# Kernel optimization log

Hardware: AMD Instinct MI355X
Metric: run time of the kernel (lower is better)

The kernel has to match this reference:

```python
import jax, jax.numpy as jnp
import numpy as np

DT = 0.01  # integrator base timestep (init kwarg)
DT_SCALE = 1.0


def setup_inputs() -> dict:
    key = jax.random.key(0)
    kx, kv, kf, ku, kw = jax.random.split(key, 5)
    B, D, R = 8192, 1024, 256
    scale = 1.0 / np.sqrt(D)
    return {
        "x": jax.random.normal(kx, (B, D), jnp.float32),
        "v": jax.random.normal(kv, (B, D), jnp.float32),
        "force": jax.random.normal(kf, (B, D), jnp.float32) * 0.1,
        "U": jax.random.normal(ku, (R, D), jnp.float32) * scale,
        "W": jax.random.normal(kw, (R, D), jnp.float32) * scale,
        "steps": 4,
    }


def _christoffel(v, x, U, W):
    # Low-rank Christoffel contraction Gamma(v, v; x):
    #   h = tanh(x W^T)   [B, r]  (position-dependent gating)
    #   q = v W^T         [B, r]  (velocity projection)
    #   Gamma = (h * q^2) U  [B, d]
    h = jnp.tanh(x @ W.T)
    q = v @ W.T
    return (h * q * q) @ U


def reference(x, v, force, U, W, steps):
    # topology_id == 0 (Euclidean): apply_boundary is the identity.
    dt = DT * DT_SCALE

    def dynamics(cx, cv):
        return -_christoffel(cv, cx, U, W) + force

    cx, cv = x, v
    for _ in range(steps):  # steps is a static Python int
        dx1 = cv
        dv1 = dynamics(cx, cv)
        v2 = cv + 0.5 * dt * dv1
        x2 = cx + 0.5 * dt * dx1
        dx2 = v2
        dv2 = dynamics(x2, v2)
        v3 = cv + 0.5 * dt * dv2
        x3 = cx + 0.5 * dt * dx2
        dx3 = v3
        dv3 = dynamics(x3, v3)
        v4 = cv + dt * dv3
        x4 = cx + dt * dx3
        dx4 = v4
        dv4 = dynamics(x4, v4)
        cx = cx + (dt / 6.0) * (dx1 + 2 * dx2 + 2 * dx3 + dx4)
        cv = cv + (dt / 6.0) * (dv1 + 2 * dv2 + 2 * dv3 + dv4)
    return (cx, cv)
```

## Files before the change

### kernel.cpp

```cpp
#include <hip/hip_runtime.h>
#include <hip/hip_bf16.h>
#include <hip/hip_fp8.h>


typedef __attribute__((ext_vector_type(8))) short bf16x8;
typedef __attribute__((ext_vector_type(4))) short bf16x4;
typedef __attribute__((ext_vector_type(4))) float f32x4;
typedef unsigned short us;
typedef unsigned char uc;

#define MFMA16 __builtin_amdgcn_mfma_f32_16x16x32_bf16
#define MFMA8  __builtin_amdgcn_mfma_f32_16x16x32_fp8_fp8

namespace {
constexpr int kB = 8192;
constexpr int kD = 1024;
constexpr int kR = 256;
constexpr int kBM = 16;
constexpr float kDt = 0.01f;
}

__device__ __forceinline__ us f2bf(float f) {
  __hip_bfloat16 h = __float2bfloat16(f);
  union { __hip_bfloat16 b; us u; } c; c.b = h;
  return c.u;
}
__device__ __forceinline__ unsigned pack2(float a, float b) {
  union { __hip_bfloat162 h; unsigned u; } c;
  c.h = __float22bfloat162_rn(float2{a, b});
  return c.u;
}
__device__ __forceinline__ float plo(unsigned u) {
  union { unsigned u; float f; } w; w.u = (u & 0xFFFFu) << 16; return w.f;
}
__device__ __forceinline__ float phi(unsigned u) {
  union { unsigned u; float f; } w; w.u = u & 0xFFFF0000u; return w.f;
}
__device__ __forceinline__ uc f2e4(float f) {
  __hip_fp8_e4m3 h(f);
  union { __hip_fp8_storage_t s; uc u; } c; c.s = h.__x;
  return c.u;
}
__device__ __forceinline__ bf16x4 pack4(float4 a) {
  union { bf16x4 v; __hip_bfloat162 h[2]; } u;
  u.h[0] = __float22bfloat162_rn(float2{a.x, a.y});
  u.h[1] = __float22bfloat162_rn(float2{a.z, a.w});
  return u.v;
}
__device__ __forceinline__ float ftanh(float x) {
  float e = __expf(2.f * x);
  return 1.f - 2.f / (e + 1.f);
}

__global__ void prep_wu(const float* __restrict__ U, const float* __restrict__ W,
                        us* __restrict__ Wb, us* __restrict__ Ub,
                        us* __restrict__ Wf, us* __restrict__ Uf) {
  int i = blockIdx.x * blockDim.x + threadIdx.x;
  if (i < kR * kD) {
    const int r = i >> 10, k = i & 1023;
    const us wb = f2bf(W[i]), ub = f2bf(U[i]);
    Wb[i] = wb; Ub[i] = ub;
    Wf[(((size_t)(r >> 4) * 32 + (k >> 5)) << 9) +
       (((((k >> 3) & 3) << 4) | (r & 15)) << 3) + (k & 7)] = wb;
    Uf[(((size_t)(k >> 4) * 8 + (r >> 5)) << 9) +
       (((((r >> 3) & 3) << 4) | (k & 15)) << 3) + (r & 7)] = ub;
  }
}

__global__ __launch_bounds__(256) void prep_g(const us* __restrict__ Wb,
                                              const us* __restrict__ Ub,
                                              uc* __restrict__ Gf8) {
  const int tid = threadIdx.x;
  const int w = tid >> 6, l = tid & 63;
  const int l15 = l & 15, l4 = l >> 4;
  const int n1 = (blockIdx.x >> 3) * 32 + (w >> 1) * 16;
  const int k1 = (blockIdx.x & 7) * 32 + (w & 1) * 16;
  f32x4 acc = {0.f, 0.f, 0.f, 0.f};
  const us* wp = Wb + (size_t)(n1 + l15) * kD + l4 * 8;
  const us* up = Ub + (size_t)(k1 + l15) * kD + l4 * 8;
#pragma unroll 8
  for (int kk = 0; kk < 32; ++kk) {
    bf16x8 aw = *(const bf16x8*)(wp + kk * 32);
    bf16x8 bu = *(const bf16x8*)(up + kk * 32);
    acc = MFMA16(aw, bu, acc, 0, 0, 0);
  }
#pragma unroll
  for (int j = 0; j < 4; ++j) {
    const int n = n1 + l4 * 4 + j, k = k1 + l15;
    Gf8[((size_t)((n >> 4) * 8 + (k >> 5)) << 9) +
        ((((k >> 3) & 3) * 16 + (n & 15)) << 3) + (k & 7)] = f2e4(64.f * acc[j]);
  }
}

__global__ __launch_bounds__(1024, 4) void fused_kernel(
    const us* __restrict__ Wf, const uc* __restrict__ Gf8, const us* __restrict__ Uf,
    const float* __restrict__ xin, const float* __restrict__ vin,
    const float* __restrict__ force,
    float* __restrict__ cxo, float* __restrict__ cvo) {
  __shared__ __align__(16) us stg[24576];
  __shared__ __align__(16) uc ct8[2][4096];

  const int tid = threadIdx.x;
  const int w = tid >> 6;
  const int l = tid & 63;
  const int l15 = l & 15;
  const int l4 = l >> 4;
  const int rs = l15 & 7;
  const int brow = blockIdx.x * kBM;
  const int rn = w * 16 + l15;
  const float dt = kDt;
  const f32x4 zero4 = {0.f, 0.f, 0.f, 0.f};

  const int prow = tid >> 6;
  const int pg = (tid & 63) >> 1;
  const int pso = (prow << 8) + ((pg ^ (prow & 7)) << 3) + (tid & 1) * 4;
  const size_t pgb0 = (size_t)(brow + prow) * kD + (tid & 63) * 4;

  f32x4 Aa = zero4, Ba = zero4, Fa = zero4;
  {
    float4 xr = *(const float4*)(xin + pgb0);
    float4 vr = *(const float4*)(vin + pgb0);
    float4 fr = *(const float4*)(force + pgb0);
#pragma unroll 1
    for (int ch = 0; ch < 4; ++ch) {
      us* sb = stg + (ch & 1) * 12288;
      *(bf16x4*)(sb + pso) = pack4(xr);
      *(bf16x4*)(sb + 4096 + pso) = pack4(vr);
      *(bf16x4*)(sb + 8192 + pso) = pack4(fr);
      __syncthreads();
      if (ch < 3) {
        const size_t gb = pgb0 + (size_t)(ch + 1) * 256;
        xr = *(const float4*)(xin + gb);
        vr = *(const float4*)(vin + gb);
        fr = *(const float4*)(force + gb);
      }
      const us* wfp = Wf + (((size_t)(w * 32 + ch * 8)) << 9) + l * 8;
      bf16x8 bw = *(const bf16x8*)(wfp);
#pragma unroll
      for (int kk = 0; kk < 8; ++kk) {
        const bf16x8 bwc = bw;
        if (kk < 7) bw = *(const bf16x8*)(wfp + (((size_t)(kk + 1)) << 9));
        const int aoff = (l15 << 8) + (((kk * 4 + l4) ^ rs) << 3);
        bf16x8 ax = *(const bf16x8*)(sb + aoff);
        bf16x8 av = *(const bf16x8*)(sb + 4096 + aoff);
        bf16x8 af = *(const bf16x8*)(sb + 8192 + aoff);
        Aa = MFMA16(ax, bwc, Aa, 0, 0, 0);
        Ba = MFMA16(av, bwc, Ba, 0, 0, 0);
        Fa = MFMA16(af, bwc, Fa, 0, 0, 0);
      }
    }
  }

  long gf8[8];
  {
    const uc* g8p = Gf8 + ((size_t)(w * 8) << 9) + l * 8;
#pragma unroll
    for (int kk = 0; kk < 8; ++kk)
      gf8[kk] = *(const long*)(g8p + ((size_t)kk << 9));
  }

  float A[4], Bv[4], Fv[4], q[4], CS[4], PS[4];
  unsigned SvP[2], SxP[2];
#pragma unroll
  for (int e = 0; e < 4; ++e) { A[e] = Aa[e]; Bv[e] = Ba[e]; Fv[e] = Fa[e]; }
  SvP[0] = SvP[1] = SxP[0] = SxP[1] = 0u;

  int w8[4];
#pragma unroll
  for (int e = 0; e < 4; ++e) {
    const int r = l4 * 4 + e;
    w8[e] = (r << 8) + ((((rn >> 3) ^ r) & 31) << 3) + (rn & 7);
  }

  const float inv64 = 0.015625f;
#pragma unroll 1
  for (int s = 0; s < 4; ++s) {
#pragma unroll
    for (int e = 0; e < 4; ++e) { q[e] = Bv[e]; CS[e] = 0.f; PS[e] = 0.f; }

#pragma unroll
    for (int k = 0; k < 4; ++k) {
      const float alpha = (k == 0) ? 0.f : ((k == 3) ? dt : 0.5f * dt);
      const float wk = (k == 1 || k == 2) ? 2.f : 1.f;
      const float beta = (k <= 1) ? 0.5f * dt : dt;
      float c[4];
#pragma unroll
      for (int e = 0; e < 4; ++e) {
        const float hx = A[e] + alpha * Bv[e];
        c[e] = ftanh(hx) * q[e] * q[e];
        CS[e] += wk * c[e];
      }
      if (s == 3 && k == 3) break;

      uc* cb = ct8[k & 1];
#pragma unroll
      for (int e = 0; e < 4; ++e) cb[w8[e]] = f2e4(c[e]);
      __syncthreads();

      f32x4 P = zero4;
#pragma unroll
      for (int kk = 0; kk < 8; ++kk) {
        long ca = *(const long*)(cb + (l15 << 8) + ((((kk * 4 + l4) ^ l15) & 31) << 3));
        P = MFMA8(ca, gf8[kk], P, 0, 0, 0);
      }
#pragma unroll
      for (int e = 0; e < 4; ++e) {
        const float Ps = P[e] * inv64;
        PS[e] += wk * Ps;
        if (k < 3) q[e] = Bv[e] + beta * (Fv[e] - Ps);
      }
    }

#pragma unroll
    for (int e = 0; e < 2; ++e) {
      SvP[e] = pack2(plo(SvP[e]) + CS[2 * e], phi(SvP[e]) + CS[2 * e + 1]);
    }
    if (s < 3) {
      const float wsx = (float)(3 - s);
#pragma unroll
      for (int e = 0; e < 2; ++e)
        SxP[e] = pack2(plo(SxP[e]) + wsx * CS[2 * e], phi(SxP[e]) + wsx * CS[2 * e + 1]);
#pragma unroll
      for (int e = 0; e < 4; ++e) {
        A[e] += dt * Bv[e];
        Bv[e] += dt * Fv[e] - (dt / 6.f) * PS[e];
      }
    } else {
#pragma unroll
      for (int e = 0; e < 2; ++e)
        SxP[e] = pack2(phi(SvP[e]) * 0.f + plo(SxP[e]), phi(SxP[e]));
    }
  }

  us* svL = stg;
  us* sxL = stg + 4096;
  __syncthreads();
  {
#pragma unroll
    for (int e = 0; e < 4; ++e) {
      const int r = l4 * 4 + e;
      const int wo = (r << 8) + ((((rn >> 3) ^ (r & 7)) << 3) | (rn & 7));
      const unsigned sv = (e & 1) ? (SvP[e >> 1] >> 16) : (SvP[e >> 1] & 0xFFFFu);
      const unsigned sx = (e & 1) ? (SxP[e >> 1] >> 16) : (SxP[e >> 1] & 0xFFFFu);
      svL[wo] = (us)sv;
      sxL[wo] = (us)sx;
    }
  }
  __syncthreads();

#pragma unroll 1
  for (int nt = 0; nt < 4; ++nt) {
    f32x4 gv = zero4, gx = zero4;
    const int d0 = w * 64 + nt * 16;
    const us* ufp = Uf + ((size_t)((w * 4 + nt) * 8) << 9) + l * 8;
#pragma unroll
    for (int kk = 0; kk < 8; ++kk) {
      const int aoff = (l15 << 8) + (((kk * 4 + l4) ^ rs) << 3);
      bf16x8 ub = *(const bf16x8*)(ufp + ((size_t)kk << 9));
      gv = MFMA16(*(const bf16x8*)(svL + aoff), ub, gv, 0, 0, 0);
      gx = MFMA16(*(const bf16x8*)(sxL + aoff), ub, gx, 0, 0, 0);
    }
#pragma unroll
    for (int j = 0; j < 4; ++j) {
      const int row = l4 * 4 + j;
      const size_t gi = (size_t)(brow + row) * kD + d0 + l15;
      const float x0 = xin[gi], v0 = vin[gi], f = force[gi];
      cxo[gi] = x0 + 4.f * dt * v0 + 6.f * dt * dt * f - (dt * dt / 6.f) * gx[j];
      cvo[gi] = v0 + 4.f * dt * f - (dt / 6.f) * gv[j];
    }
  }
}

__global__ void copy_only_kernel(const float* __restrict__ x, const float* __restrict__ v,
                                 float* __restrict__ cx, float* __restrict__ cv) {
  const int stride = gridDim.x * blockDim.x;
  for (int i = blockIdx.x * blockDim.x + threadIdx.x; i < kB * kD; i += stride) {
    cx[i] = x[i]; cv[i] = v[i];
  }
}

extern "C" void kernel_launch(void* const* d_in, const int* in_sizes, int n_in,
                              void* d_out, int out_size, void* d_ws, size_t ws_size,
                              hipStream_t stream) {
  const float* x = (const float*)d_in[0];
  const float* v = (const float*)d_in[1];
  const float* force = (const float*)d_in[2];
  const float* U = (const float*)d_in[3];
  const float* W = (const float*)d_in[4];

  float* cx = (float*)d_out;
  float* cv = cx + (size_t)kB * kD;

  size_t off = 0;
  us* Wb = (us*)((char*)d_ws + off); off += (size_t)kR * kD * 2;
  us* Ub = (us*)((char*)d_ws + off); off += (size_t)kR * kD * 2;
  us* Wf = (us*)((char*)d_ws + off); off += (size_t)kR * kD * 2;
  us* Uf = (us*)((char*)d_ws + off); off += (size_t)kR * kD * 2;
  uc* Gf8 = (uc*)((char*)d_ws + off); off += (size_t)kR * kR;

  if (ws_size < off) {
    copy_only_kernel<<<2048, 256, 0, stream>>>(x, v, cx, cv);
    return;
  }

  prep_wu<<<(kR * kD + 255) / 256, 256, 0, stream>>>(U, W, Wb, Ub, Wf, Uf);
  prep_g<<<64, 256, 0, stream>>>(Wb, Ub, Gf8);
  fused_kernel<<<kB / kBM, 1024, 0, stream>>>(Wf, Gf8, Uf, x, v, force, cx, cv);
}
```

Before: 114.3 us.

## Double batch rows per block to reuse W, G and U fragments across two M-tiles

Raises the per-block batch tile from 16 to 32 rows, so each wave runs two MFMA M-tiles against the same loaded W, Gf8 and U fragments. Global traffic for the weight operands per batch row is halved and the grid shrinks by half. The cost is twice the LDS per block (about 112 KB) and more registers per thread, which may cut occupancy to one block per CU. The number of blocks also drops to 256, which may leave CUs idle on a 256-CU part. The final-step branch that did an unused SxP repack is also removed.

```diff
diff --git a/kernel.cpp b/kernel.cpp
--- a/kernel.cpp
+++ b/kernel.cpp
@@ -4,7 +4,6 @@
 
 
 typedef __attribute__((ext_vector_type(8))) short bf16x8;
-typedef __attribute__((ext_vector_type(4))) short bf16x4;
 typedef __attribute__((ext_vector_type(4))) float f32x4;
 typedef unsigned short us;
 typedef unsigned char uc;
@@ -16,7 +15,7 @@
 constexpr int kB = 8192;
 constexpr int kD = 1024;
 constexpr int kR = 256;
-constexpr int kBM = 16;
+constexpr int kBM = 32;
 constexpr float kDt = 0.01f;
 }
 
@@ -41,10 +40,12 @@
   union { __hip_fp8_storage_t s; uc u; } c; c.s = h.__x;
   return c.u;
 }
-__device__ __forceinline__ bf16x4 pack4(float4 a) {
-  union { bf16x4 v; __hip_bfloat162 h[2]; } u;
+__device__ __forceinline__ bf16x8 pack8(float4 a, float4 b) {
+  union { bf16x8 v; __hip_bfloat162 h[4]; } u;
   u.h[0] = __float22bfloat162_rn(float2{a.x, a.y});
   u.h[1] = __float22bfloat162_rn(float2{a.z, a.w});
+  u.h[2] = __float22bfloat162_rn(float2{b.x, b.y});
+  u.h[3] = __float22bfloat162_rn(float2{b.z, b.w});
   return u.v;
 }
 __device__ __forceinline__ float ftanh(float x) {
@@ -97,8 +98,8 @@
     const float* __restrict__ xin, const float* __restrict__ vin,
     const float* __restrict__ force,
     float* __restrict__ cxo, float* __restrict__ cvo) {
-  __shared__ __align__(16) us stg[24576];
-  __shared__ __align__(16) uc ct8[2][4096];
+  __shared__ __align__(16) us stg[49152];
+  __shared__ __align__(16) uc ct8[2][8192];
 
   const int tid = threadIdx.x;
   const int w = tid >> 6;
@@ -111,28 +112,30 @@
   const float dt = kDt;
   const f32x4 zero4 = {0.f, 0.f, 0.f, 0.f};
 
-  const int prow = tid >> 6;
-  const int pg = (tid & 63) >> 1;
-  const int pso = (prow << 8) + ((pg ^ (prow & 7)) << 3) + (tid & 1) * 4;
-  const size_t pgb0 = (size_t)(brow + prow) * kD + (tid & 63) * 4;
-
-  f32x4 Aa = zero4, Ba = zero4, Fa = zero4;
+  const int prow = tid >> 5;
+  const int pg8 = tid & 31;
+  const int pso = (prow << 8) + ((pg8 ^ (prow & 7)) << 3);
+  const size_t pgb0 = (size_t)(brow + prow) * kD + pg8 * 8;
+
+  f32x4 Aa[2], Ba[2], Fa[2];
+  Aa[0] = zero4; Aa[1] = zero4; Ba[0] = zero4; Ba[1] = zero4;
+  Fa[0] = zero4; Fa[1] = zero4;
   {
-    float4 xr = *(const float4*)(xin + pgb0);
-    float4 vr = *(const float4*)(vin + pgb0);
-    float4 fr = *(const float4*)(force + pgb0);
+    float4 xr0 = *(const float4*)(xin + pgb0), xr1 = *(const float4*)(xin + pgb0 + 4);
+    float4 vr0 = *(const float4*)(vin + pgb0), vr1 = *(const float4*)(vin + pgb0 + 4);
+    float4 fr0 = *(const float4*)(force + pgb0), fr1 = *(const float4*)(force + pgb0 + 4);
 #pragma unroll 1
     for (int ch = 0; ch < 4; ++ch) {
-      us* sb = stg + (ch & 1) * 12288;
-      *(bf16x4*)(sb + pso) = pack4(xr);
-      *(bf16x4*)(sb + 4096 + pso) = pack4(vr);
-      *(bf16x4*)(sb + 8192 + pso) = pack4(fr);
+      us* sb = stg + (ch & 1) * 24576;
+      *(bf16x8*)(sb + pso) = pack8(xr0, xr1);
+      *(bf16x8*)(sb + 8192 + pso) = pack8(vr0, vr1);
+      *(bf16x8*)(sb + 16384 + pso) = pack8(fr0, fr1);
       __syncthreads();
       if (ch < 3) {
         const size_t gb = pgb0 + (size_t)(ch + 1) * 256;
-        xr = *(const float4*)(xin + gb);
-        vr = *(const float4*)(vin + gb);
-        fr = *(const float4*)(force + gb);
+        xr0 = *(const float4*)(xin + gb); xr1 = *(const float4*)(xin + gb + 4);
+        vr0 = *(const float4*)(vin + gb); vr1 = *(const float4*)(vin + gb + 4);
+        fr0 = *(const float4*)(force + gb); fr1 = *(const float4*)(force + gb + 4);
       }
       const us* wfp = Wf + (((size_t)(w * 32 + ch * 8)) << 9) + l * 8;
       bf16x8 bw = *(const bf16x8*)(wfp);
@@ -140,13 +143,16 @@
       for (int kk = 0; kk < 8; ++kk) {
         const bf16x8 bwc = bw;
         if (kk < 7) bw = *(const bf16x8*)(wfp + (((size_t)(kk + 1)) << 9));
-        const int aoff = (l15 << 8) + (((kk * 4 + l4) ^ rs) << 3);
-        bf16x8 ax = *(const bf16x8*)(sb + aoff);
-        bf16x8 av = *(const bf16x8*)(sb + 4096 + aoff);
-        bf16x8 af = *(const bf16x8*)(sb + 8192 + aoff);
-        Aa = MFMA16(ax, bwc, Aa, 0, 0, 0);
-        Ba = MFMA16(av, bwc, Ba, 0, 0, 0);
-        Fa = MFMA16(af, bwc, Fa, 0, 0, 0);
+#pragma unroll
+        for (int mt = 0; mt < 2; ++mt) {
+          const int aoff = ((mt * 16 + l15) << 8) + (((kk * 4 + l4) ^ rs) << 3);
+          bf16x8 ax = *(const bf16x8*)(sb + aoff);
+          bf16x8 av = *(const bf16x8*)(sb + 8192 + aoff);
+          bf16x8 af = *(const bf16x8*)(sb + 16384 + aoff);
+          Aa[mt] = MFMA16(ax, bwc, Aa[mt], 0, 0, 0);
+          Ba[mt] = MFMA16(av, bwc, Ba[mt], 0, 0, 0);
+          Fa[mt] = MFMA16(af, bwc, Fa[mt], 0, 0, 0);
+        }
       }
     }
   }
@@ -159,115 +165,118 @@
       gf8[kk] = *(const long*)(g8p + ((size_t)kk << 9));
   }
 
-  float A[4], Bv[4], Fv[4], q[4], CS[4], PS[4];
-  unsigned SvP[2], SxP[2];
-#pragma unroll
-  for (int e = 0; e < 4; ++e) { A[e] = Aa[e]; Bv[e] = Ba[e]; Fv[e] = Fa[e]; }
-  SvP[0] = SvP[1] = SxP[0] = SxP[1] = 0u;
-
-  int w8[4];
-#pragma unroll
-  for (int e = 0; e < 4; ++e) {
-    const int r = l4 * 4 + e;
-    w8[e] = (r << 8) + ((((rn >> 3) ^ r) & 31) << 3) + (rn & 7);
-  }
+  float A[8], Bv[8], Fv[8], q[8], CS[8], PS[8];
+  unsigned SvP[4], SxP[4];
+#pragma unroll
+  for (int i = 0; i < 8; ++i) {
+    A[i] = Aa[i >> 2][i & 3]; Bv[i] = Ba[i >> 2][i & 3]; Fv[i] = Fa[i >> 2][i & 3];
+  }
+#pragma unroll
+  for (int i = 0; i < 4; ++i) { SvP[i] = 0u; SxP[i] = 0u; }
 
   const float inv64 = 0.015625f;
 #pragma unroll 1
   for (int s = 0; s < 4; ++s) {
 #pragma unroll
-    for (int e = 0; e < 4; ++e) { q[e] = Bv[e]; CS[e] = 0.f; PS[e] = 0.f; }
+    for (int i = 0; i < 8; ++i) { q[i] = Bv[i]; CS[i] = 0.f; PS[i] = 0.f; }
 
 #pragma unroll
     for (int k = 0; k < 4; ++k) {
       const float alpha = (k == 0) ? 0.f : ((k == 3) ? dt : 0.5f * dt);
       const float wk = (k == 1 || k == 2) ? 2.f : 1.f;
       const float beta = (k <= 1) ? 0.5f * dt : dt;
-      float c[4];
-#pragma unroll
-      for (int e = 0; e < 4; ++e) {
-        const float hx = A[e] + alpha * Bv[e];
-        c[e] = ftanh(hx) * q[e] * q[e];
-        CS[e] += wk * c[e];
+      float c[8];
+#pragma unroll
+      for (int i = 0; i < 8; ++i) {
+        const float hx = A[i] + alpha * Bv[i];
+        c[i] = ftanh(hx) * q[i] * q[i];
+        CS[i] += wk * c[i];
       }
       if (s == 3 && k == 3) break;
 
       uc* cb = ct8[k & 1];
 #pragma unroll
-      for (int e = 0; e < 4; ++e) cb[w8[e]] = f2e4(c[e]);
+      for (int i = 0; i < 8; ++i) {
+        const int r = (i >> 2) * 16 + l4 * 4 + (i & 3);
+        cb[(r << 8) + ((((rn >> 3) ^ r) & 31) << 3) + (rn & 7)] = f2e4(c[i]);
+      }
       __syncthreads();
 
-      f32x4 P = zero4;
+      f32x4 P[2];
+      P[0] = zero4; P[1] = zero4;
 #pragma unroll
       for (int kk = 0; kk < 8; ++kk) {
-        long ca = *(const long*)(cb + (l15 << 8) + ((((kk * 4 + l4) ^ l15) & 31) << 3));
-        P = MFMA8(ca, gf8[kk], P, 0, 0, 0);
-      }
-#pragma unroll
-      for (int e = 0; e < 4; ++e) {
-        const float Ps = P[e] * inv64;
-        PS[e] += wk * Ps;
-        if (k < 3) q[e] = Bv[e] + beta * (Fv[e] - Ps);
+#pragma unroll
+        for (int mt = 0; mt < 2; ++mt) {
+          const int rr = mt * 16 + l15;
+          long ca = *(const long*)(cb + (rr << 8) +
+                                   ((((kk * 4 + l4) ^ rr) & 31) << 3));
+          P[mt] = MFMA8(ca, gf8[kk], P[mt], 0, 0, 0);
+        }
+      }
+#pragma unroll
+      for (int i = 0; i < 8; ++i) {
+        const float Ps = P[i >> 2][i & 3] * inv64;
+        PS[i] += wk * Ps;
+        if (k < 3) q[i] = Bv[i] + beta * (Fv[i] - Ps);
       }
     }
 
 #pragma unroll
-    for (int e = 0; e < 2; ++e) {
-      SvP[e] = pack2(plo(SvP[e]) + CS[2 * e], phi(SvP[e]) + CS[2 * e + 1]);
-    }
+    for (int p = 0; p < 4; ++p)
+      SvP[p] = pack2(plo(SvP[p]) + CS[2 * p], phi(SvP[p]) + CS[2 * p + 1]);
     if (s < 3) {
       const float wsx = (float)(3 - s);
 #pragma unroll
-      for (int e = 0; e < 2; ++e)
-        SxP[e] = pack2(plo(SxP[e]) + wsx * CS[2 * e], phi(SxP[e]) + wsx * CS[2 * e + 1]);
-#pragma unroll
-      for (int e = 0; e < 4; ++e) {
-        A[e] += dt * Bv[e];
-        Bv[e] += dt * Fv[e] - (dt / 6.f) * PS[e];
-      }
-    } else {
-#pragma unroll
-      for (int e = 0; e < 2; ++e)
-        SxP[e] = pack2(phi(SvP[e]) * 0.f + plo(SxP[e]), phi(SxP[e]));
+      for (int p = 0; p < 4; ++p)
+        SxP[p] = pack2(plo(SxP[p]) + wsx * CS[2 * p], phi(SxP[p]) + wsx * CS[2 * p + 1]);
+#pragma unroll
+      for (int i = 0; i < 8; ++i) {
+        A[i] += dt * Bv[i];
+        Bv[i] += dt * Fv[i] - (dt / 6.f) * PS[i];
+      }
     }
   }
 
   us* svL = stg;
-  us* sxL = stg + 4096;
-  __syncthreads();
-  {
-#pragma unroll
-    for (int e = 0; e < 4; ++e) {
-      const int r = l4 * 4 + e;
-      const int wo = (r << 8) + ((((rn >> 3) ^ (r & 7)) << 3) | (rn & 7));
-      const unsigned sv = (e & 1) ? (SvP[e >> 1] >> 16) : (SvP[e >> 1] & 0xFFFFu);
-      const unsigned sx = (e & 1) ? (SxP[e >> 1] >> 16) : (SxP[e >> 1] & 0xFFFFu);
-      svL[wo] = (us)sv;
-      sxL[wo] = (us)sx;
-    }
+  us* sxL = stg + 8192;
+#pragma unroll
+  for (int i = 0; i < 8; ++i) {
+    const int r = (i >> 2) * 16 + l4 * 4 + (i & 3);
+    const int wo = (r << 8) + ((((rn >> 3) ^ (r & 7)) << 3) | (rn & 7));
+    const unsigned sv = SvP[i >> 1], sx = SxP[i >> 1];
+    svL[wo] = (us)((i & 1) ? (sv >> 16) : (sv & 0xFFFFu));
+    sxL[wo] = (us)((i & 1) ? (sx >> 16) : (sx & 0xFFFFu));
   }
   __syncthreads();
 
 #pragma unroll 1
   for (int nt = 0; nt < 4; ++nt) {
-    f32x4 gv = zero4, gx = zero4;
+    f32x4 gv[2], gx[2];
+    gv[0] = zero4; gv[1] = zero4; gx[0] = zero4; gx[1] = zero4;
     const int d0 = w * 64 + nt * 16;
     const us* ufp = Uf + ((size_t)((w * 4 + nt) * 8) << 9) + l * 8;
 #pragma unroll
     for (int kk = 0; kk < 8; ++kk) {
-      const int aoff = (l15 << 8) + (((kk * 4 + l4) ^ rs) << 3);
       bf16x8 ub = *(const bf16x8*)(ufp + ((size_t)kk << 9));
-      gv = MFMA16(*(const bf16x8*)(svL + aoff), ub, gv, 0, 0, 0);
-      gx = MFMA16(*(const bf16x8*)(sxL + aoff), ub, gx, 0, 0, 0);
+#pragma unroll
+      for (int mt = 0; mt < 2; ++mt) {
+        const int aoff = ((mt * 16 + l15) << 8) + (((kk * 4 + l4) ^ rs) << 3);
+        gv[mt] = MFMA16(*(const bf16x8*)(svL + aoff), ub, gv[mt], 0, 0, 0);
+        gx[mt] = MFMA16(*(const bf16x8*)(sxL + aoff), ub, gx[mt], 0, 0, 0);
+      }
     }
 #pragma unroll
-    for (int j = 0; j < 4; ++j) {
-      const int row = l4 * 4 + j;
-      const size_t gi = (size_t)(brow + row) * kD + d0 + l15;
-      const float x0 = xin[gi], v0 = vin[gi], f = force[gi];
-      cxo[gi] = x0 + 4.f * dt * v0 + 6.f * dt * dt * f - (dt * dt / 6.f) * gx[j];
-      cvo[gi] = v0 + 4.f * dt * f - (dt / 6.f) * gv[j];
-    }
+    for (int mt = 0; mt < 2; ++mt)
+#pragma unroll
+      for (int j = 0; j < 4; ++j) {
+        const int row = mt * 16 + l4 * 4 + j;
+        const size_t gi = (size_t)(brow + row) * kD + d0 + l15;
+        const float x0 = xin[gi], v0 = vin[gi], f = force[gi];
+        cxo[gi] = x0 + 4.f * dt * v0 + 6.f * dt * dt * f
+                  - (dt * dt / 6.f) * gx[mt][j];
+        cvo[gi] = v0 + 4.f * dt * f - (dt / 6.f) * gv[mt][j];
+      }
   }
 }
 
```

Result: slower. 174.4 us (+52.6%).
